# Optimization experiments

Hardware: AMD Instinct MI355X
Metric: run time of the kernel (lower is better)

The kernel has to match this reference:

```python
import jax, jax.numpy as jnp
import numpy as np

LOG2PI = 1.8378770664093453


def setup_inputs() -> dict:
    key = jax.random.key(0)
    ks = jax.random.split(key, 8)
    B, IN, OUT = 16384, 2048, 1
    x = jax.random.normal(ks[0], (B, IN), dtype=jnp.float32)
    y = jax.random.normal(ks[1], (B, OUT), dtype=jnp.float32)
    counter = jax.random.uniform(ks[2], (B,), dtype=jnp.float32)
    # learned params (flax init: zeros / normal(stddev=0.01) / normal/in_features)
    noise_mean = jnp.zeros((OUT,), dtype=jnp.float32)
    noise_logdiag = 0.01 * jax.random.normal(ks[3], (OUT,), dtype=jnp.float32)
    W_mean = 0.01 * jax.random.normal(ks[4], (OUT, IN), dtype=jnp.float32)
    W_logdiag = 0.01 * jax.random.normal(ks[5], (OUT, IN), dtype=jnp.float32)
    W_offdiag = jax.random.normal(ks[6], (OUT, IN, IN), dtype=jnp.float32) / IN
    return {"x": x, "y": y, "counter": counter,
            "noise_mean": noise_mean, "noise_logdiag": noise_logdiag,
            "W_mean": W_mean, "W_logdiag": W_logdiag, "W_offdiag": W_offdiag}


def reference(x, y, counter, noise_mean, noise_logdiag, W_mean, W_logdiag, W_offdiag):
    # hyperparams matching init_kwargs
    regularization_weight = 0.0001
    prior_scale = 1.0
    wishart_scale = 0.01
    dof = 1.0
    in_f = x.shape[-1]
    out_f = W_mean.shape[0]
    adjusted_dof = (dof + out_f + 1.0) / 2.0

    # Cholesky factor of W covariance: strict lower triangle + exp(logdiag) on diag
    L = jnp.tril(W_offdiag, k=-1) + jnp.exp(W_logdiag)[..., None] * jnp.eye(in_f, dtype=x.dtype)  # (out,in,in)

    # predictive mean under W_mean; diagonal noise
    pred_mean = x @ W_mean.T  # (B,out)
    pred_likelihood = (-0.5 * ((y - pred_mean) / jnp.exp(noise_logdiag)) ** 2
                       - noise_logdiag - 0.5 * LOG2PI)  # (B,out) elementwise Gaussian logpdf

    # covariance-weighted inner product: (L^T b)^2 summed, b = counter-scaled x
    x_mod = x * counter[:, None]  # (B,in)
    Ltb = jnp.einsum('oij,bi->boj', L, x_mod)  # (B,out,in)
    quad = jnp.sum(Ltb * Ltb, axis=-1)  # (B,out) = b^T L L^T b per out
    noise_prec = jnp.exp(-2.0 * noise_logdiag)  # (out,)
    trace_term = 0.5 * quad * noise_prec  # (B,out)

    # KL(q(W) || N(0, prior_scale I))
    mse_term = jnp.sum(W_mean ** 2) / prior_scale
    trace_cov = jnp.sum(L * L, axis=(-1, -2))  # (out,)
    logdet_cov = 2.0 * jnp.sum(W_logdiag, axis=-1)  # (out,)
    kl_term = 0.5 * (mse_term + jnp.sum(trace_cov) / prior_scale
                     + jnp.sum(in_f * jnp.log(prior_scale) - logdet_cov))

    # Wishart prior terms on noise precision
    logdet_precision = jnp.sum(-2.0 * noise_logdiag)
    trace_precision = jnp.sum(noise_prec)
    wishart_term = adjusted_dof * logdet_precision - 0.5 * wishart_scale * trace_precision

    total_elbo = jnp.sum((pred_likelihood.squeeze() - trace_term.squeeze()) * counter) / jnp.sum(counter)
    total_elbo = total_elbo + regularization_weight * (wishart_term - kl_term)
    return -total_elbo
```

## Files before the change

### kernel.cpp

```cpp
#include <hip/hip_runtime.h>
#include <hip/hip_bf16.h>
#include <math.h>

#define LOG2PI_F 1.8378770664093453f

typedef int i32x4 __attribute__((ext_vector_type(4)));
typedef int i32x8 __attribute__((ext_vector_type(8)));
typedef float f32x4 __attribute__((ext_vector_type(4)));

#define M_DIM 16384
#define K_DIM 2048
#define N_DIM 2048
#define BM 256
#define BN 256
#define BK 128
#define NB_N (N_DIM / BN)
#define NB_M (M_DIM / BM)
#define LSCALE 256.0f
#define QDESCALE (1.0f / 65536.0f)
#define SCALE_ONE 0x7F7F7F7F

__device__ __forceinline__ void gload16(const void* g, void* l) {
    __builtin_amdgcn_global_load_lds(
        (__attribute__((address_space(1))) void*)g,
        (__attribute__((address_space(3))) void*)l, 16, 0, 0);
}

__device__ __forceinline__ unsigned int pk4_fp8(float a, float b, float c, float d) {
    unsigned int w = (unsigned int)__builtin_amdgcn_cvt_pk_fp8_f32(a, b, 0, false);
    w = (unsigned int)__builtin_amdgcn_cvt_pk_fp8_f32(c, d, (int)w, true);
    return w;
}

__global__ __launch_bounds__(256) void build_Lt(const float* __restrict__ Woff,
                                                const float* __restrict__ Wld,
                                                unsigned char* __restrict__ Lq,
                                                float* __restrict__ misc_arr) {
    __shared__ float tile[64][65];
    __shared__ float red[4];
    const int jt = blockIdx.x * 64;
    const int it = blockIdx.y * 64;
    const int tid = threadIdx.x;
    float ss = 0.f;

    if (it + 63 >= jt) {
        for (int e = tid; e < 4096; e += 256) {
            int r = e >> 6, c = e & 63;
            tile[r][c] = Woff[(size_t)(it + r) * K_DIM + (jt + c)];
        }
    }
    __syncthreads();

    for (int e = tid; e < 4096; e += 256) {
        int jr = e >> 6, ic = e & 63;
        int i = it + ic, j = jt + jr;
        float v = 0.f;
        if (i > j) {
            v = tile[ic][jr];
            ss += v * v;
        } else if (i == j) {
            v = expf(Wld[i]);
        }
        unsigned int w = (unsigned int)__builtin_amdgcn_cvt_pk_fp8_f32(v * LSCALE, 0.f, 0, false);
        Lq[(size_t)j * K_DIM + i] = (unsigned char)(w & 0xffu);
    }

    #pragma unroll
    for (int off = 32; off; off >>= 1) ss += __shfl_down(ss, off);
    if ((tid & 63) == 0) red[tid >> 6] = ss;
    __syncthreads();
    if (tid == 0)
        misc_arr[blockIdx.y * 32 + blockIdx.x] = red[0] + red[1] + red[2] + red[3];
}

__global__ __launch_bounds__(256) void prep_x(const float* __restrict__ X,
                                              const float* __restrict__ Wm,
                                              unsigned char* __restrict__ Xq,
                                              float* __restrict__ U) {
    const int b = blockIdx.x;
    const int tid = threadIdx.x;
    const float* xr = X + (size_t)b * K_DIM;
    unsigned char* xo = Xq + (size_t)b * K_DIM;
    __shared__ float red[4];
    const int base = tid * 8;
    float4 v0 = *(const float4*)(xr + base);
    float4 v1 = *(const float4*)(xr + base + 4);
    float4 w0 = *(const float4*)(Wm + base);
    float4 w1 = *(const float4*)(Wm + base + 4);
    float dot = v0.x * w0.x + v0.y * w0.y + v0.z * w0.z + v0.w * w0.w
              + v1.x * w1.x + v1.y * w1.y + v1.z * w1.z + v1.w * w1.w;
    uint2 p;
    p.x = pk4_fp8(v0.x, v0.y, v0.z, v0.w);
    p.y = pk4_fp8(v1.x, v1.y, v1.z, v1.w);
    *(uint2*)(xo + base) = p;
    #pragma unroll
    for (int off = 32; off; off >>= 1) dot += __shfl_down(dot, off);
    if ((tid & 63) == 0) red[tid >> 6] = dot;
    __syncthreads();
    if (tid == 0) U[b] = red[0] + red[1] + red[2] + red[3];
}

__device__ __forceinline__ i32x8 frag128(const unsigned char* base, int roff, int g) {
    const unsigned char* rb = base + roff * 128;
    int x = (roff & 7) << 4;
    i32x4 lo = *(const i32x4*)(rb + (((g * 2) << 4) ^ x));
    i32x4 hi = *(const i32x4*)(rb + (((g * 2 + 1) << 4) ^ x));
    return __builtin_shufflevector(lo, hi, 0, 1, 2, 3, 4, 5, 6, 7);
}

#define MXMFMA(A, B, C) __builtin_amdgcn_mfma_scale_f32_16x16x128_f8f6f4( \
        (A), (B), (C), 0, 0, 0, SCALE_ONE, 0, SCALE_ONE)

#define BAR() asm volatile("s_barrier" ::: "memory")
#define WAITL() { asm volatile("s_waitcnt lgkmcnt(0)" ::: "memory"); \
                  __builtin_amdgcn_sched_barrier(0); }

__global__ __launch_bounds__(512, 2) void quad_gemm(const unsigned char* __restrict__ Xq,
                                                    const unsigned char* __restrict__ Lq,
                                                    float* __restrict__ qpart) {
    __shared__ unsigned char As[2][BM * BK];
    __shared__ unsigned char Bs[2][BN * BK];

    const int mb = blockIdx.x;
    const int jp = blockIdx.y;
    const int tid = threadIdx.x;
    const int lane = tid & 63;
    const int wid = tid >> 6;
    const int wr = wid >> 2, wc = wid & 3;
    const int g = lane >> 4, r16 = lane & 15;
    const int brow = mb * BM;

    const int srow = lane >> 3;
    const int scol = (lane & 7) ^ srow;

    auto gemm_one = [&](int nb) {
        const int bcol = nb * BN;
        const int NT = (K_DIM - bcol) >> 7;

        const unsigned char* pA[2];
        const unsigned char* pB[2];
        #pragma unroll
        for (int h = 0; h < 2; ++h) {
            pA[h] = Xq + (size_t)(brow + h * 128 + wid * 16 + srow) * K_DIM + bcol + scol * 16;
            pB[h] = Lq + (size_t)(bcol + h * 128 + wid * 16 + srow) * K_DIM + bcol + scol * 16;
        }

        auto stgA = [&](int t, int h, int buf) {
            const unsigned char* s = pA[h] + (size_t)t * 128;
            char* d = (char*)As[buf] + h * 16384 + wid * 2048;
            gload16(s, d);
            gload16(s + (size_t)8 * K_DIM, d + 1024);
        };
        auto stgB = [&](int t, int h, int buf) {
            const unsigned char* s = pB[h] + (size_t)t * 128;
            char* d = (char*)Bs[buf] + h * 16384 + wid * 2048;
            gload16(s, d);
            gload16(s + (size_t)8 * K_DIM, d + 1024);
        };

        f32x4 acc[8][4];
        const f32x4 zero = {0.f, 0.f, 0.f, 0.f};
        #pragma unroll
        for (int m = 0; m < 8; ++m)
            #pragma unroll
            for (int n = 0; n < 4; ++n) acc[m][n] = zero;

        stgA(0, 0, 0); stgA(0, 1, 0); stgB(0, 0, 0); stgB(0, 1, 0);
        stgB(1, 0, 1); stgB(1, 1, 1);
        asm volatile("s_waitcnt vmcnt(4)" ::: "memory");
        BAR();

        for (int t = 0; t < NT; ++t) {
            const int cur = t & 1, nbuf = cur ^ 1;
            const unsigned char* Abase = As[cur] + wr * 16384;
            const unsigned char* Bbase = Bs[cur] + (wc >> 1) * 16384;
            const int brow2 = (wc & 1) * 64;
            const bool s1 = (t + 1 < NT), s2 = (t + 2 < NT);
            i32x8 bf[4], af[4];

            #pragma unroll
            for (int n = 0; n < 4; ++n) bf[n] = frag128(Bbase, brow2 + n * 16 + r16, g);
            #pragma unroll
            for (int m = 0; m < 4; ++m) af[m] = frag128(Abase, m * 16 + r16, g);
            if (s1) { stgA(t + 1, 0, nbuf); stgA(t + 1, 1, nbuf); }
            BAR();
            WAITL();
            __builtin_amdgcn_s_setprio(1);
            #pragma unroll
            for (int m = 0; m < 4; ++m)
                #pragma unroll
                for (int n = 0; n < 4; ++n)
                    acc[m][n] = MXMFMA(af[m], bf[n], acc[m][n]);
            __builtin_amdgcn_s_setprio(0);
            BAR();

            #pragma unroll
            for (int m = 0; m < 4; ++m) af[m] = frag128(Abase, 64 + m * 16 + r16, g);
            if (s2) { stgB(t + 2, 0, cur); stgB(t + 2, 1, cur); }
            BAR();
            WAITL();
            __builtin_amdgcn_s_setprio(1);
            #pragma unroll
            for (int m = 0; m < 4; ++m)
                #pragma unroll
                for (int n = 0; n < 4; ++n)
                    acc[4 + m][n] = MXMFMA(af[m], bf[n], acc[4 + m][n]);
            __builtin_amdgcn_s_setprio(0);

            if (s2)
                asm volatile("s_waitcnt vmcnt(4)" ::: "memory");
            else if (s1)
                asm volatile("s_waitcnt vmcnt(0)" ::: "memory");
            BAR();
        }

        float* qbuf = (float*)&As[0][0];
        __syncthreads();
        #pragma unroll
        for (int m = 0; m < 8; ++m) {
            #pragma unroll
            for (int r = 0; r < 4; ++r) {
                float s = 0.f;
                #pragma unroll
                for (int n = 0; n < 4; ++n) {
                    float t = acc[m][n][r];
                    s += t * t;
                }
                #pragma unroll
                for (int off = 1; off < 16; off <<= 1) s += __shfl_xor(s, off);
                if (r16 == 0) qbuf[wc * 256 + wr * 128 + m * 16 + g * 4 + r] = s;
            }
        }
        __syncthreads();
        if (tid < BM)
            qpart[(size_t)(brow + tid) * NB_N + nb] =
                (qbuf[tid] + qbuf[256 + tid] + qbuf[512 + tid] + qbuf[768 + tid]) * QDESCALE;
        __syncthreads();
    };

    gemm_one(jp);
    gemm_one(7 - jp);
}
#undef BAR
#undef WAITL

__global__ __launch_bounds__(256) void row_part(const float* __restrict__ Y,
                                                const float* __restrict__ Cnt,
                                                const float* __restrict__ nld_p,
                                                const float* __restrict__ U,
                                                const float* __restrict__ qpart,
                                                double* __restrict__ dpart) {
    const int tid = threadIdx.x;
    const float nld = nld_p[0];
    const float inv_sig = expf(-nld);
    const float nprec = inv_sig * inv_sig;
    double s1 = 0.0, s2 = 0.0;
    const int base = blockIdx.x * 512;
    #pragma unroll
    for (int j = 0; j < 2; ++j) {
        int b = base + j * 256 + tid;
        float c = Cnt[b];
        const float4* qp = (const float4*)(qpart + (size_t)b * NB_N);
        float4 q0 = qp[0], q1 = qp[1];
        float q = q0.x + q0.y + q0.z + q0.w + q1.x + q1.y + q1.z + q1.w;
        float d = (Y[b] - U[b]) * inv_sig;
        float pl = -0.5f * d * d - nld - 0.5f * LOG2PI_F;
        float tt = 0.5f * q * c * c * nprec;
        s1 += (double)c;
        s2 += (double)((pl - tt) * c);
    }
    __shared__ double red[2][4];
    #pragma unroll
    for (int off = 32; off; off >>= 1) {
        s1 += __shfl_down(s1, off);
        s2 += __shfl_down(s2, off);
    }
    if ((tid & 63) == 0) { red[0][tid >> 6] = s1; red[1][tid >> 6] = s2; }
    __syncthreads();
    if (tid == 0) {
        dpart[blockIdx.x * 2 + 0] = red[0][0] + red[0][1] + red[0][2] + red[0][3];
        dpart[blockIdx.x * 2 + 1] = red[1][0] + red[1][1] + red[1][2] + red[1][3];
    }
}

__global__ __launch_bounds__(256) void finalize2(const float* __restrict__ nld_p,
                                                 const float* __restrict__ Wm,
                                                 const float* __restrict__ Wld,
                                                 const double* __restrict__ dpart,
                                                 const float* __restrict__ misc_arr,
                                                 float* __restrict__ out) {
    const int tid = threadIdx.x;
    const float nld = nld_p[0];
    const float inv_sig = expf(-nld);
    const float nprec = inv_sig * inv_sig;

    double s1 = 0.0, s2 = 0.0;
    if (tid < 32) { s1 = dpart[tid * 2]; s2 = dpart[tid * 2 + 1]; }

    double wm2 = 0.0, tcd = 0.0, wls = 0.0, offs = 0.0;
    for (int i = tid; i < K_DIM; i += 256) {
        float w = Wm[i];
        wm2 += (double)w * (double)w;
        float ld = Wld[i];
        tcd += exp(2.0 * (double)ld);
        wls += (double)ld;
    }
    for (int i = tid; i < 1024; i += 256) offs += (double)misc_arr[i];

    __shared__ double red[6][4];
    double vals[6] = {s1, s2, wm2, tcd, wls, offs};
    #pragma unroll
    for (int s = 0; s < 6; ++s) {
        double v = vals[s];
        #pragma unroll
        for (int off = 32; off; off >>= 1) v += __shfl_down(v, off);
        if ((tid & 63) == 0) red[s][tid >> 6] = v;
    }
    __syncthreads();
    if (tid == 0) {
        double S1 = red[0][0] + red[0][1] + red[0][2] + red[0][3];
        double S2 = red[1][0] + red[1][1] + red[1][2] + red[1][3];
        double MSE = red[2][0] + red[2][1] + red[2][2] + red[2][3];
        double TCD = red[3][0] + red[3][1] + red[3][2] + red[3][3];
        double WLS = red[4][0] + red[4][1] + red[4][2] + red[4][3];
        double OFFS = red[5][0] + red[5][1] + red[5][2] + red[5][3];

        double trace_cov = OFFS + TCD;
        double kl = 0.5 * (MSE + trace_cov - 2.0 * WLS);
        double wish = 1.5 * (-2.0 * (double)nld) - 0.005 * (double)nprec;
        double elbo = S2 / S1 + 1e-4 * (wish - kl);
        out[0] = (float)(-elbo);
    }
}

extern "C" void kernel_launch(void* const* d_in, const int* in_sizes, int n_in,
                              void* d_out, int out_size, void* d_ws, size_t ws_size,
                              hipStream_t stream) {
    const float* x    = (const float*)d_in[0];
    const float* y    = (const float*)d_in[1];
    const float* cnt  = (const float*)d_in[2];
    const float* nld  = (const float*)d_in[4];
    const float* Wm   = (const float*)d_in[5];
    const float* Wld  = (const float*)d_in[6];
    const float* Woff = (const float*)d_in[7];

    char* ws = (char*)d_ws;
    unsigned char* Xq = (unsigned char*)(ws);
    unsigned char* Lq = (unsigned char*)(ws + 33554432);
    double* dpart  = (double*)(ws + 40000000);
    float*  U      = (float*)(ws + 75497472);
    float*  qpart  = (float*)(ws + 75563008);
    float*  misc   = (float*)(ws + 76611584);

    build_Lt<<<dim3(32, 32), 256, 0, stream>>>(Woff, Wld, Lq, misc);
    prep_x<<<dim3(M_DIM), 256, 0, stream>>>(x, Wm, Xq, U);
    quad_gemm<<<dim3(NB_M, 4), 512, 0, stream>>>(Xq, Lq, qpart);
    row_part<<<dim3(32), 256, 0, stream>>>(y, cnt, nld, U, qpart, dpart);
    finalize2<<<1, 256, 0, stream>>>(nld, Wm, Wld, dpart, misc, (float*)d_out);
}
```

Before: 98.13 us.

## Shrink quad GEMM tiles to 128x128 with simpler double-buffered pipeline

Reduces the FP8 quad GEMM tile from 256x256 with 512 threads to 128x128 with 256 threads, and doubles the grid along the column-block dimension. The two-phase split-K-half schedule with separate A/B staging two steps ahead is replaced by a plain one-step-ahead double buffer that stages A and B together. The intent is more, smaller blocks so the triangular work balances better and occupancy rises. In exchange each block does less reuse per LDS byte and the prefetch is only one stage deep, with a full vmcnt(0) wait each iteration.

Measured after the change: 101.5 us. +3.4%, slower.

```diff
diff --git a/kernel.cpp b/kernel.cpp
--- a/kernel.cpp
+++ b/kernel.cpp
@@ -11,8 +11,8 @@
 #define M_DIM 16384
 #define K_DIM 2048
 #define N_DIM 2048
-#define BM 256
-#define BN 256
+#define BM 128
+#define BN 128
 #define BK 128
 #define NB_N (N_DIM / BN)
 #define NB_M (M_DIM / BM)
@@ -112,10 +112,8 @@
         (A), (B), (C), 0, 0, 0, SCALE_ONE, 0, SCALE_ONE)
 
 #define BAR() asm volatile("s_barrier" ::: "memory")
-#define WAITL() { asm volatile("s_waitcnt lgkmcnt(0)" ::: "memory"); \
-                  __builtin_amdgcn_sched_barrier(0); }
-
-__global__ __launch_bounds__(512, 2) void quad_gemm(const unsigned char* __restrict__ Xq,
+
+__global__ __launch_bounds__(256, 2) void quad_gemm(const unsigned char* __restrict__ Xq,
                                                     const unsigned char* __restrict__ Lq,
                                                     float* __restrict__ qpart) {
     __shared__ unsigned char As[2][BM * BK];
@@ -126,7 +124,7 @@
     const int tid = threadIdx.x;
     const int lane = tid & 63;
     const int wid = tid >> 6;
-    const int wr = wid >> 2, wc = wid & 3;
+    const int wr = wid >> 1, wc = wid & 1;
     const int g = lane >> 4, r16 = lane & 15;
     const int brow = mb * BM;
 
@@ -137,54 +135,47 @@
         const int bcol = nb * BN;
         const int NT = (K_DIM - bcol) >> 7;
 
-        const unsigned char* pA[2];
-        const unsigned char* pB[2];
-        #pragma unroll
-        for (int h = 0; h < 2; ++h) {
-            pA[h] = Xq + (size_t)(brow + h * 128 + wid * 16 + srow) * K_DIM + bcol + scol * 16;
-            pB[h] = Lq + (size_t)(bcol + h * 128 + wid * 16 + srow) * K_DIM + bcol + scol * 16;
-        }
-
-        auto stgA = [&](int t, int h, int buf) {
-            const unsigned char* s = pA[h] + (size_t)t * 128;
-            char* d = (char*)As[buf] + h * 16384 + wid * 2048;
-            gload16(s, d);
-            gload16(s + (size_t)8 * K_DIM, d + 1024);
+        const unsigned char* pA =
+            Xq + (size_t)(brow + wid * 32 + srow) * K_DIM + bcol + scol * 16;
+        const unsigned char* pB =
+            Lq + (size_t)(bcol + wid * 32 + srow) * K_DIM + bcol + scol * 16;
+
+        auto stage = [&](int t, int buf) {
+            const unsigned char* sa = pA + (size_t)t * 128;
+            const unsigned char* sb = pB + (size_t)t * 128;
+            char* da = (char*)As[buf] + wid * 4096;
+            char* db = (char*)Bs[buf] + wid * 4096;
+            #pragma unroll
+            for (int j = 0; j < 4; ++j) {
+                gload16(sa + (size_t)(j * 8) * K_DIM, da + j * 1024);
+                gload16(sb + (size_t)(j * 8) * K_DIM, db + j * 1024);
+            }
         };
-        auto stgB = [&](int t, int h, int buf) {
-            const unsigned char* s = pB[h] + (size_t)t * 128;
-            char* d = (char*)Bs[buf] + h * 16384 + wid * 2048;
-            gload16(s, d);
-            gload16(s + (size_t)8 * K_DIM, d + 1024);
-        };
-
-        f32x4 acc[8][4];
+
+        f32x4 acc[4][4];
         const f32x4 zero = {0.f, 0.f, 0.f, 0.f};
         #pragma unroll
-        for (int m = 0; m < 8; ++m)
+        for (int m = 0; m < 4; ++m)
             #pragma unroll
             for (int n = 0; n < 4; ++n) acc[m][n] = zero;
 
-        stgA(0, 0, 0); stgA(0, 1, 0); stgB(0, 0, 0); stgB(0, 1, 0);
-        stgB(1, 0, 1); stgB(1, 1, 1);
-        asm volatile("s_waitcnt vmcnt(4)" ::: "memory");
+        stage(0, 0);
+        asm volatile("s_waitcnt vmcnt(0)" ::: "memory");
         BAR();
 
         for (int t = 0; t < NT; ++t) {
             const int cur = t & 1, nbuf = cur ^ 1;
-            const unsigned char* Abase = As[cur] + wr * 16384;
-            const unsigned char* Bbase = Bs[cur] + (wc >> 1) * 16384;
-            const int brow2 = (wc & 1) * 64;
-            const bool s1 = (t + 1 < NT), s2 = (t + 2 < NT);
-            i32x8 bf[4], af[4];
-
-            #pragma unroll
-            for (int n = 0; n < 4; ++n) bf[n] = frag128(Bbase, brow2 + n * 16 + r16, g);
-            #pragma unroll
-            for (int m = 0; m < 4; ++m) af[m] = frag128(Abase, m * 16 + r16, g);
-            if (s1) { stgA(t + 1, 0, nbuf); stgA(t + 1, 1, nbuf); }
-            BAR();
-            WAITL();
+            const unsigned char* Ab = As[cur];
+            const unsigned char* Bb = Bs[cur];
+            const bool s1 = (t + 1 < NT);
+            if (s1) stage(t + 1, nbuf);
+
+            i32x8 af[4], bf[4];
+            #pragma unroll
+            for (int n = 0; n < 4; ++n) bf[n] = frag128(Bb, wc * 64 + n * 16 + r16, g);
+            #pragma unroll
+            for (int m = 0; m < 4; ++m) af[m] = frag128(Ab, wr * 64 + m * 16 + r16, g);
+
             __builtin_amdgcn_s_setprio(1);
             #pragma unroll
             for (int m = 0; m < 4; ++m)
@@ -192,24 +183,8 @@
                 for (int n = 0; n < 4; ++n)
                     acc[m][n] = MXMFMA(af[m], bf[n], acc[m][n]);
             __builtin_amdgcn_s_setprio(0);
-            BAR();
-
-            #pragma unroll
-            for (int m = 0; m < 4; ++m) af[m] = frag128(Abase, 64 + m * 16 + r16, g);
-            if (s2) { stgB(t + 2, 0, cur); stgB(t + 2, 1, cur); }
-            BAR();
-            WAITL();
-            __builtin_amdgcn_s_setprio(1);
-            #pragma unroll
-            for (int m = 0; m < 4; ++m)
-                #pragma unroll
-                for (int n = 0; n < 4; ++n)
-                    acc[4 + m][n] = MXMFMA(af[m], bf[n], acc[4 + m][n]);
-            __builtin_amdgcn_s_setprio(0);
-
-            if (s2)
-                asm volatile("s_waitcnt vmcnt(4)" ::: "memory");
-            else if (s1)
+
+            if (s1)
                 asm volatile("s_waitcnt vmcnt(0)" ::: "memory");
             BAR();
         }
@@ -217,7 +192,7 @@
         float* qbuf = (float*)&As[0][0];
         __syncthreads();
         #pragma unroll
-        for (int m = 0; m < 8; ++m) {
+        for (int m = 0; m < 4; ++m) {
             #pragma unroll
             for (int r = 0; r < 4; ++r) {
                 float s = 0.f;
@@ -228,21 +203,20 @@
                 }
                 #pragma unroll
                 for (int off = 1; off < 16; off <<= 1) s += __shfl_xor(s, off);
-                if (r16 == 0) qbuf[wc * 256 + wr * 128 + m * 16 + g * 4 + r] = s;
+                if (r16 == 0) qbuf[wc * 128 + wr * 64 + m * 16 + g * 4 + r] = s;
             }
         }
         __syncthreads();
         if (tid < BM)
             qpart[(size_t)(brow + tid) * NB_N + nb] =
-                (qbuf[tid] + qbuf[256 + tid] + qbuf[512 + tid] + qbuf[768 + tid]) * QDESCALE;
+                (qbuf[tid] + qbuf[128 + tid]) * QDESCALE;
         __syncthreads();
     };
 
     gemm_one(jp);
-    gemm_one(7 - jp);
+    gemm_one(15 - jp);
 }
 #undef BAR
-#undef WAITL
 
 __global__ __launch_bounds__(256) void row_part(const float* __restrict__ Y,
                                                 const float* __restrict__ Cnt,
@@ -261,8 +235,12 @@
         int b = base + j * 256 + tid;
         float c = Cnt[b];
         const float4* qp = (const float4*)(qpart + (size_t)b * NB_N);
-        float4 q0 = qp[0], q1 = qp[1];
-        float q = q0.x + q0.y + q0.z + q0.w + q1.x + q1.y + q1.z + q1.w;
+        float q = 0.f;
+        #pragma unroll
+        for (int v4 = 0; v4 < 4; ++v4) {
+            float4 qv = qp[v4];
+            q += qv.x + qv.y + qv.z + qv.w;
+        }
         float d = (Y[b] - U[b]) * inv_sig;
         float pl = -0.5f * d * d - nld - 0.5f * LOG2PI_F;
         float tt = 0.5f * q * c * c * nprec;
@@ -354,7 +332,7 @@
 
     build_Lt<<<dim3(32, 32), 256, 0, stream>>>(Woff, Wld, Lq, misc);
     prep_x<<<dim3(M_DIM), 256, 0, stream>>>(x, Wm, Xq, U);
-    quad_gemm<<<dim3(NB_M, 4), 512, 0, stream>>>(Xq, Lq, qpart);
+    quad_gemm<<<dim3(NB_M, 8), 256, 0, stream>>>(Xq, Lq, qpart);
     row_part<<<dim3(32), 256, 0, stream>>>(y, cnt, nld, U, qpart, dpart);
     finalize2<<<1, 256, 0, stream>>>(nld, Wm, Wld, dpart, misc, (float*)d_out);
 }
```
